# Performance work log

Measured on AMD Instinct MI355X. Metric: run time of the kernel, lower is better.

The kernel has to match this reference:

```python
import jax, jax.numpy as jnp
import numpy as np

T, B, M = 512, 4096, 2
DT = 1.0
HARD_RESET = True


def setup_inputs() -> dict:
    key = jax.random.key(0)
    ks = jax.random.split(key, 8)
    x_seq = jax.random.normal(ks[0], (T, B), jnp.float32) * 0.5
    w = jax.random.normal(ks[1], (B, B), jnp.float32) * (0.5 / np.sqrt(B))
    b = jax.random.normal(ks[2], (B,), jnp.float32) * 0.1
    v0 = jnp.zeros((B,), jnp.float32)
    Iasc0 = jnp.zeros((B, M), jnp.float32)
    v_th = jnp.ones((B,), jnp.float32)
    v_reset = jnp.zeros((B,), jnp.float32)
    v_rest = jnp.zeros((B,), jnp.float32)
    c_m = jnp.ones((B,), jnp.float32)
    tau = jax.random.uniform(ks[3], (B,), jnp.float32, 5.0, 20.0)
    k = jax.random.uniform(ks[4], (B, M), jnp.float32, 0.1, 0.5)
    asc = jax.random.normal(ks[5], (B, M), jnp.float32) * 0.1
    mask = jnp.ones((B,), jnp.float32)
    return dict(x_seq=x_seq, w=w, b=b, v0=v0, Iasc0=Iasc0, v_th=v_th,
                v_reset=v_reset, v_rest=v_rest, c_m=c_m, tau=tau, k=k,
                asc=asc, mask=mask)


def reference(x_seq, w, b, v0, Iasc0, v_th, v_reset, v_rest, c_m, tau, k, asc, mask):
    a = jnp.exp(-DT / tau)                 # (B,) voltage decay
    bdec = jnp.exp(-k * DT)                # (B,M) ASC decay

    def step(carry, x_t):
        v, I, s_prev = carry
        I_sum = I.sum(-1)                  # (B,)
        lin = w @ s_prev                   # recurrent GEMV against prev spikes
        x = x_t + b + lin
        v_inf = v_rest + tau * (x + I_sum) / c_m
        v_p = v_inf + (v - v_inf) * a
        u = (v_p - v_th) / (v_th - v_reset)
        s = (u > 0.0).astype(v_p.dtype) * mask
        if HARD_RESET:
            v_post = v_p - (v_p - v_reset) * s
        else:
            v_post = v_p - (v_th - v_reset) * s
        I_new = I * bdec + asc * s[:, None]
        return (v_post, I_new, s), (s, v_post)

    (v_fin, I_fin, _), (s_seq, v_seq) = jax.lax.scan(
        step, (v0, Iasc0, jnp.zeros_like(v0)), x_seq)
    return s_seq, v_seq, v_fin, I_fin
```

## Files before the change

kernel.cpp:

```cpp
#include <hip/hip_runtime.h>
#include <math.h>

#define TSTEPS 512
#define BN 4096
#define NBLK 64
#define NTHR 512
#define NPB 64
#define NWAVE 8
#define ESTRIDE 16

typedef unsigned long long u64;

__device__ __forceinline__ u64 ld_agent(const u64* p) {
    return __hip_atomic_load(p, __ATOMIC_RELAXED, __HIP_MEMORY_SCOPE_AGENT);
}
__device__ __forceinline__ void st_agent(u64* p, u64 v) {
    __hip_atomic_store(p, v, __ATOMIC_RELAXED, __HIP_MEMORY_SCOPE_AGENT);
}

template<bool TR>
__global__ __launch_bounds__(NTHR, 1)
void glif_kernel(const float* __restrict__ x_seq, const float* __restrict__ w,
                 const float* __restrict__ b_in, const float* __restrict__ v0,
                 const float* __restrict__ Ia0, const float* __restrict__ vth_in,
                 const float* __restrict__ vrst_in, const float* __restrict__ vrest_in,
                 const float* __restrict__ cm_in, const float* __restrict__ tau_in,
                 const float* __restrict__ k_in, const float* __restrict__ asc_in,
                 const float* __restrict__ mask_in,
                 float* __restrict__ out_s, float* __restrict__ out_v,
                 float* __restrict__ out_vf, float* __restrict__ out_if,
                 u64* __restrict__ sbuf, unsigned* __restrict__ bar,
                 float* __restrict__ wT)
{
    __shared__ float  tile[64][65];
    __shared__ int    wlist[NWAVE][512];
    __shared__ float4 partials[2][NWAVE][16];

    const int blk = blockIdx.x;
    const int tid = threadIdx.x;
    const int n0 = blk * NPB;
    const int wv = tid >> 6;
    const int ln = tid & 63;

    if (TR) {
        for (int tt = 0; tt < 64; ++tt) {
            int tile_id = blk + tt * NBLK;
            int ti = tile_id >> 6, tj = tile_id & 63;
            int c = tid & 63, r0 = tid >> 6;
#pragma unroll
            for (int rr = 0; rr < 8; ++rr) {
                int r = r0 + rr * 8;
                tile[r][c] = w[(size_t)(ti * 64 + r) * BN + tj * 64 + c];
            }
            __syncthreads();
            int rw = tid & 63, c0 = tid >> 6;
#pragma unroll
            for (int cc = 0; cc < 8; ++cc) {
                int cw = c0 + cc * 8;
                float mcol = mask_in[tj * 64 + cw];
                wT[(size_t)(tj * 64 + cw) * BN + ti * 64 + rw] = tile[rw][cw] * mcol;
            }
            __syncthreads();
        }
    }

    __syncthreads();
    if (tid == 0) {
        __threadfence();
        __hip_atomic_fetch_add(bar, 1u, __ATOMIC_ACQ_REL, __HIP_MEMORY_SCOPE_AGENT);
        while (__hip_atomic_load(bar, __ATOMIC_RELAXED, __HIP_MEMORY_SCOPE_AGENT) < NBLK) {
            __builtin_amdgcn_s_sleep(8);
        }
        __threadfence();
    }
    __syncthreads();

    const int n = n0 + tid;
    float v = 0, I0 = 0, I1 = 0, bb = 0, aa = 0, bd0 = 0, bd1 = 0, as0 = 0, as1 = 0,
          vth = 0, vrst = 0, vrest = 0, cm = 1, tau = 1, msk = 0;
    if (tid < NPB) {
        v = v0[n]; I0 = Ia0[2 * n]; I1 = Ia0[2 * n + 1];
        bb = b_in[n]; vth = vth_in[n]; vrst = vrst_in[n]; vrest = vrest_in[n];
        cm = cm_in[n]; tau = tau_in[n]; msk = mask_in[n];
        aa  = (float)exp((double)(-1.0f / tau));
        bd0 = (float)exp((double)(-k_in[2 * n]));
        bd1 = (float)exp((double)(-k_in[2 * n + 1]));
        as0 = asc_in[2 * n]; as1 = asc_in[2 * n + 1];
    }

    const int e = ln >> 3;
    const int sub = ln & 7;
    const int wsel = sub >> 2;
    const int bshift = 8 * (sub & 3);
    const int cbase = ((wv * 8 + e) << 6) + (sub << 3);

    const int cslot = ln >> 4, l16 = ln & 15;
    const float* wb4 = wT + n0 + l16 * 4;

    for (int t = 0; t < TSTEPS; ++t) {
        float xt = 0.0f;
        if (tid < NPB) xt = x_seq[(size_t)t * BN + n];

        const u64* p = sbuf + ((size_t)(t & 1) * NBLK + (wv * 8 + e)) * ESTRIDE + wsel;
        const unsigned want = (unsigned)t;
        u64 ev = ld_agent(p);
        while ((unsigned)(ev >> 32) != want) {
            __builtin_amdgcn_s_sleep(1);
            ev = ld_agent(p);
        }
        unsigned byte = ((unsigned)ev >> bshift) & 0xFFu;

        int c = __popc(byte);
        int x = c;
#pragma unroll
        for (int d = 1; d < 64; d <<= 1) {
            int y = __shfl_up(x, d);
            if (ln >= d) x += y;
        }
        const int kw = __shfl(x, 63);
        int base = x - c;
        while (byte) { int bp = __ffs(byte) - 1; byte &= byte - 1; wlist[wv][base++] = cbase + bp; }

        float4 acc = make_float4(0.f, 0.f, 0.f, 0.f);
        const int R = (kw + 3) >> 2;
        if (TR) {
            for (int r = 0; r < R; r += 8) {
#pragma unroll
                for (int u = 0; u < 8; ++u) {
                    int idx = (r + u) * 4 + cslot;
                    bool pg = idx < kw;
                    int j = wlist[wv][pg ? idx : 0];
                    float m = pg ? 1.0f : 0.0f;
                    const float4 wvv = *reinterpret_cast<const float4*>(wb4 + ((size_t)j << 12));
                    acc.x = fmaf(wvv.x, m, acc.x);
                    acc.y = fmaf(wvv.y, m, acc.y);
                    acc.z = fmaf(wvv.z, m, acc.z);
                    acc.w = fmaf(wvv.w, m, acc.w);
                }
            }
#pragma unroll
            for (int d = 16; d < 64; d <<= 1) {
                acc.x += __shfl_xor(acc.x, d);
                acc.y += __shfl_xor(acc.y, d);
                acc.z += __shfl_xor(acc.z, d);
                acc.w += __shfl_xor(acc.w, d);
            }
            if (ln < 16) partials[t & 1][wv][ln] = acc;
        } else {
            float accs = 0.f;
            const float* wrow = w + (size_t)(n0 + ln) * BN;
            for (int i = 0; i < kw; ++i) {
                int j = wlist[wv][i];
                accs = fmaf(wrow[j], mask_in[j], accs);
            }
            reinterpret_cast<float*>(&partials[t & 1][wv][0])[ln] = accs;
        }
        __syncthreads();

        float s = 0.0f;
        if (tid < NPB) {
            const float* pf = reinterpret_cast<const float*>(&partials[t & 1][0][0]);
            float l0 = pf[tid],        l1 = pf[64 + tid],  l2 = pf[128 + tid], l3 = pf[192 + tid];
            float l4 = pf[256 + tid],  l5 = pf[320 + tid], l6 = pf[384 + tid], l7 = pf[448 + tid];
            float lin = ((l0 + l1) + (l2 + l3)) + ((l4 + l5) + (l6 + l7));
            float xx = (xt + bb) + lin;
            float Isum = I0 + I1;
            float vinf = vrest + (tau * (xx + Isum)) / cm;
            float vp = vinf + (v - vinf) * aa;
            float uu = (vp - vth) / (vth - vrst);
            s = (uu > 0.0f) ? msk : 0.0f;
            u64 bal = __ballot(s != 0.0f);
            if (tid == 0) {
                u64 tagw = ((u64)(t + 1)) << 32;
                u64* dst = sbuf + ((size_t)((t + 1) & 1) * NBLK + blk) * ESTRIDE;
                st_agent(dst,     tagw | (u64)(unsigned)bal);
                st_agent(dst + 1, tagw | (u64)(unsigned)(bal >> 32));
            }
            float vpost = vp - (vp - vrst) * s;
            I0 = I0 * bd0 + as0 * s;
            I1 = I1 * bd1 + as1 * s;
            v = vpost;
            out_s[(size_t)t * BN + n] = s;
            out_v[(size_t)t * BN + n] = vpost;
        }
    }

    if (tid < NPB) {
        out_vf[n] = v;
        out_if[2 * n] = I0;
        out_if[2 * n + 1] = I1;
    }
}

extern "C" void kernel_launch(void* const* d_in, const int* in_sizes, int n_in,
                              void* d_out, int out_size, void* d_ws, size_t ws_size,
                              hipStream_t stream)
{
    const float* x_seq = (const float*)d_in[0];
    const float* w     = (const float*)d_in[1];
    const float* b     = (const float*)d_in[2];
    const float* v0    = (const float*)d_in[3];
    const float* Ia0   = (const float*)d_in[4];
    const float* vth   = (const float*)d_in[5];
    const float* vrst  = (const float*)d_in[6];
    const float* vrest = (const float*)d_in[7];
    const float* cm    = (const float*)d_in[8];
    const float* tau   = (const float*)d_in[9];
    const float* k     = (const float*)d_in[10];
    const float* asc   = (const float*)d_in[11];
    const float* mask  = (const float*)d_in[12];

    float* out_s  = (float*)d_out;
    float* out_v  = out_s + (size_t)TSTEPS * BN;
    float* out_vf = out_v + (size_t)TSTEPS * BN;
    float* out_if = out_vf + BN;

    const size_t mb_bytes = (size_t)2 * NBLK * ESTRIDE * sizeof(u64);
    u64* sbuf     = (u64*)d_ws;
    unsigned* bar = (unsigned*)((char*)d_ws + mb_bytes);
    float* wT     = (float*)((char*)d_ws + mb_bytes + 256);

    const size_t need = mb_bytes + 256 + (size_t)BN * BN * sizeof(float);
    const bool tr = (ws_size >= need);

    hipMemsetAsync(d_ws, 0, mb_bytes + 256, stream);

    if (tr) {
        glif_kernel<true><<<NBLK, NTHR, 0, stream>>>(
            x_seq, w, b, v0, Ia0, vth, vrst, vrest, cm, tau, k, asc, mask,
            out_s, out_v, out_vf, out_if, sbuf, bar, wT);
    } else {
        glif_kernel<false><<<NBLK, NTHR, 0, stream>>>(
            x_seq, w, b, v0, Ia0, vth, vrst, vrest, cm, tau, k, asc, mask,
            out_s, out_v, out_vf, out_if, sbuf, bar, (float*)w);
    }
}
```

Before: 1.708 ms.

## Split into a dedicated neuron-update wave and eight gather waves using LDS flags

Adds a ninth wave that owns the per-neuron state update and spike broadcast. The eight gather waves now signal completion through workgroup-scope release/acquire flags in LDS instead of a block-wide __syncthreads each timestep, and partials become a four-deep ring so gather waves can run ahead. The spin-wait on the global spike buffer also issues two loads per iteration with no sleep, to cut polling latency. The goal is to take the block barrier off the per-step critical path, at the cost of busy-spinning in LDS and in global memory.

```diff
diff --git a/kernel.cpp b/kernel.cpp
--- a/kernel.cpp
+++ b/kernel.cpp
@@ -4,9 +4,9 @@
 #define TSTEPS 512
 #define BN 4096
 #define NBLK 64
-#define NTHR 512
+#define NTHR 576
 #define NPB 64
-#define NWAVE 8
+#define NGW 8
 #define ESTRIDE 16
 
 typedef unsigned long long u64;
@@ -16,6 +16,12 @@
 }
 __device__ __forceinline__ void st_agent(u64* p, u64 v) {
     __hip_atomic_store(p, v, __ATOMIC_RELAXED, __HIP_MEMORY_SCOPE_AGENT);
+}
+__device__ __forceinline__ void st_flag(unsigned* p, unsigned v) {
+    __hip_atomic_store(p, v, __ATOMIC_RELEASE, __HIP_MEMORY_SCOPE_WORKGROUP);
+}
+__device__ __forceinline__ unsigned ld_flag(const unsigned* p) {
+    return __hip_atomic_load(p, __ATOMIC_ACQUIRE, __HIP_MEMORY_SCOPE_WORKGROUP);
 }
 
 template<bool TR>
@@ -32,9 +38,10 @@
                  u64* __restrict__ sbuf, unsigned* __restrict__ bar,
                  float* __restrict__ wT)
 {
-    __shared__ float  tile[64][65];
-    __shared__ int    wlist[NWAVE][512];
-    __shared__ float4 partials[2][NWAVE][16];
+    __shared__ float    tile[64][65];
+    __shared__ int      wlist[NGW][512];
+    __shared__ float4   partials[4][NGW][16];
+    __shared__ unsigned flags[NGW];
 
     const int blk = blockIdx.x;
     const int tid = threadIdx.x;
@@ -46,23 +53,29 @@
         for (int tt = 0; tt < 64; ++tt) {
             int tile_id = blk + tt * NBLK;
             int ti = tile_id >> 6, tj = tile_id & 63;
-            int c = tid & 63, r0 = tid >> 6;
-#pragma unroll
-            for (int rr = 0; rr < 8; ++rr) {
-                int r = r0 + rr * 8;
-                tile[r][c] = w[(size_t)(ti * 64 + r) * BN + tj * 64 + c];
+            if (tid < 512) {
+                int c = tid & 63, r0 = tid >> 6;
+#pragma unroll
+                for (int rr = 0; rr < 8; ++rr) {
+                    int r = r0 + rr * 8;
+                    tile[r][c] = w[(size_t)(ti * 64 + r) * BN + tj * 64 + c];
+                }
             }
             __syncthreads();
-            int rw = tid & 63, c0 = tid >> 6;
-#pragma unroll
-            for (int cc = 0; cc < 8; ++cc) {
-                int cw = c0 + cc * 8;
-                float mcol = mask_in[tj * 64 + cw];
-                wT[(size_t)(tj * 64 + cw) * BN + ti * 64 + rw] = tile[rw][cw] * mcol;
+            if (tid < 512) {
+                int rw = tid & 63, c0 = tid >> 6;
+#pragma unroll
+                for (int cc = 0; cc < 8; ++cc) {
+                    int cw = c0 + cc * 8;
+                    float mcol = mask_in[tj * 64 + cw];
+                    wT[(size_t)(tj * 64 + cw) * BN + ti * 64 + rw] = tile[rw][cw] * mcol;
+                }
             }
             __syncthreads();
         }
     }
+
+    if (tid < NGW) flags[tid] = 0;
 
     __syncthreads();
     if (tid == 0) {
@@ -75,10 +88,9 @@
     }
     __syncthreads();
 
-    const int n = n0 + tid;
-    float v = 0, I0 = 0, I1 = 0, bb = 0, aa = 0, bd0 = 0, bd1 = 0, as0 = 0, as1 = 0,
-          vth = 0, vrst = 0, vrest = 0, cm = 1, tau = 1, msk = 0;
-    if (tid < NPB) {
+    if (wv == 0) {
+        const int n = n0 + ln;
+        float v, I0, I1, bb, aa, bd0, bd1, as0, as1, vth, vrst, vrest, cm, tau, msk;
         v = v0[n]; I0 = Ia0[2 * n]; I1 = Ia0[2 * n + 1];
         bb = b_in[n]; vth = vth_in[n]; vrst = vrst_in[n]; vrest = vrest_in[n];
         cm = cm_in[n]; tau = tau_in[n]; msk = mask_in[n];
@@ -86,96 +98,28 @@
         bd0 = (float)exp((double)(-k_in[2 * n]));
         bd1 = (float)exp((double)(-k_in[2 * n + 1]));
         as0 = asc_in[2 * n]; as1 = asc_in[2 * n + 1];
-    }
-
-    const int e = ln >> 3;
-    const int sub = ln & 7;
-    const int wsel = sub >> 2;
-    const int bshift = 8 * (sub & 3);
-    const int cbase = ((wv * 8 + e) << 6) + (sub << 3);
-
-    const int cslot = ln >> 4, l16 = ln & 15;
-    const float* wb4 = wT + n0 + l16 * 4;
-
-    for (int t = 0; t < TSTEPS; ++t) {
-        float xt = 0.0f;
-        if (tid < NPB) xt = x_seq[(size_t)t * BN + n];
-
-        const u64* p = sbuf + ((size_t)(t & 1) * NBLK + (wv * 8 + e)) * ESTRIDE + wsel;
-        const unsigned want = (unsigned)t;
-        u64 ev = ld_agent(p);
-        while ((unsigned)(ev >> 32) != want) {
-            __builtin_amdgcn_s_sleep(1);
-            ev = ld_agent(p);
-        }
-        unsigned byte = ((unsigned)ev >> bshift) & 0xFFu;
-
-        int c = __popc(byte);
-        int x = c;
-#pragma unroll
-        for (int d = 1; d < 64; d <<= 1) {
-            int y = __shfl_up(x, d);
-            if (ln >= d) x += y;
-        }
-        const int kw = __shfl(x, 63);
-        int base = x - c;
-        while (byte) { int bp = __ffs(byte) - 1; byte &= byte - 1; wlist[wv][base++] = cbase + bp; }
-
-        float4 acc = make_float4(0.f, 0.f, 0.f, 0.f);
-        const int R = (kw + 3) >> 2;
-        if (TR) {
-            for (int r = 0; r < R; r += 8) {
-#pragma unroll
-                for (int u = 0; u < 8; ++u) {
-                    int idx = (r + u) * 4 + cslot;
-                    bool pg = idx < kw;
-                    int j = wlist[wv][pg ? idx : 0];
-                    float m = pg ? 1.0f : 0.0f;
-                    const float4 wvv = *reinterpret_cast<const float4*>(wb4 + ((size_t)j << 12));
-                    acc.x = fmaf(wvv.x, m, acc.x);
-                    acc.y = fmaf(wvv.y, m, acc.y);
-                    acc.z = fmaf(wvv.z, m, acc.z);
-                    acc.w = fmaf(wvv.w, m, acc.w);
-                }
-            }
-#pragma unroll
-            for (int d = 16; d < 64; d <<= 1) {
-                acc.x += __shfl_xor(acc.x, d);
-                acc.y += __shfl_xor(acc.y, d);
-                acc.z += __shfl_xor(acc.z, d);
-                acc.w += __shfl_xor(acc.w, d);
-            }
-            if (ln < 16) partials[t & 1][wv][ln] = acc;
-        } else {
-            float accs = 0.f;
-            const float* wrow = w + (size_t)(n0 + ln) * BN;
-            for (int i = 0; i < kw; ++i) {
-                int j = wlist[wv][i];
-                accs = fmaf(wrow[j], mask_in[j], accs);
-            }
-            reinterpret_cast<float*>(&partials[t & 1][wv][0])[ln] = accs;
-        }
-        __syncthreads();
-
-        float s = 0.0f;
-        if (tid < NPB) {
-            const float* pf = reinterpret_cast<const float*>(&partials[t & 1][0][0]);
-            float l0 = pf[tid],        l1 = pf[64 + tid],  l2 = pf[128 + tid], l3 = pf[192 + tid];
-            float l4 = pf[256 + tid],  l5 = pf[320 + tid], l6 = pf[384 + tid], l7 = pf[448 + tid];
+
+        for (int t = 0; t < TSTEPS; ++t) {
+            float xt = x_seq[(size_t)t * BN + n];
+
+            if (ln < NGW) {
+                const unsigned want = (unsigned)(t + 1);
+                while (ld_flag(&flags[ln]) < want) {}
+            }
+            const float* pf = reinterpret_cast<const float*>(&partials[t & 3][0][0]);
+            float l0 = pf[ln],        l1 = pf[64 + ln],  l2 = pf[128 + ln], l3 = pf[192 + ln];
+            float l4 = pf[256 + ln],  l5 = pf[320 + ln], l6 = pf[384 + ln], l7 = pf[448 + ln];
             float lin = ((l0 + l1) + (l2 + l3)) + ((l4 + l5) + (l6 + l7));
             float xx = (xt + bb) + lin;
             float Isum = I0 + I1;
             float vinf = vrest + (tau * (xx + Isum)) / cm;
             float vp = vinf + (v - vinf) * aa;
             float uu = (vp - vth) / (vth - vrst);
-            s = (uu > 0.0f) ? msk : 0.0f;
+            float s = (uu > 0.0f) ? msk : 0.0f;
             u64 bal = __ballot(s != 0.0f);
-            if (tid == 0) {
-                u64 tagw = ((u64)(t + 1)) << 32;
-                u64* dst = sbuf + ((size_t)((t + 1) & 1) * NBLK + blk) * ESTRIDE;
-                st_agent(dst,     tagw | (u64)(unsigned)bal);
-                st_agent(dst + 1, tagw | (u64)(unsigned)(bal >> 32));
-            }
+            u64 tagw = ((u64)(t + 1)) << 32;
+            u64* dst = sbuf + ((size_t)((t + 1) & 1) * NBLK + blk) * ESTRIDE;
+            if (ln < 2) st_agent(dst + ln, tagw | (u64)(unsigned)(bal >> (32 * ln)));
             float vpost = vp - (vp - vrst) * s;
             I0 = I0 * bd0 + as0 * s;
             I1 = I1 * bd1 + as1 * s;
@@ -183,12 +127,79 @@
             out_s[(size_t)t * BN + n] = s;
             out_v[(size_t)t * BN + n] = vpost;
         }
-    }
-
-    if (tid < NPB) {
         out_vf[n] = v;
         out_if[2 * n] = I0;
         out_if[2 * n + 1] = I1;
+    } else {
+        const int gw = wv - 1;
+        const int e = ln >> 3;
+        const int sub = ln & 7;
+        const int wsel = sub >> 2;
+        const int bshift = 8 * (sub & 3);
+        const int entry = gw * 8 + e;
+        const int cbase = (entry << 6) + (sub << 3);
+        const int cslot = ln >> 4, l16 = ln & 15;
+        const float* wb4 = wT + n0 + l16 * 4;
+
+        for (int t = 0; t < TSTEPS; ++t) {
+            const u64* p = sbuf + ((size_t)(t & 1) * NBLK + entry) * ESTRIDE + wsel;
+            const unsigned want = (unsigned)t;
+            u64 ev;
+            for (;;) {
+                u64 A = ld_agent(p);
+                u64 B = ld_agent(p);
+                if ((unsigned)(A >> 32) == want) { ev = A; break; }
+                if ((unsigned)(B >> 32) == want) { ev = B; break; }
+            }
+            unsigned byte = ((unsigned)ev >> bshift) & 0xFFu;
+
+            int c = __popc(byte);
+            int x = c;
+#pragma unroll
+            for (int d = 1; d < 64; d <<= 1) {
+                int y = __shfl_up(x, d);
+                if (ln >= d) x += y;
+            }
+            const int kw = __shfl(x, 63);
+            int base = x - c;
+            while (byte) { int bp = __ffs(byte) - 1; byte &= byte - 1; wlist[gw][base++] = cbase + bp; }
+
+            if (TR) {
+                float4 acc = make_float4(0.f, 0.f, 0.f, 0.f);
+                const int R = (kw + 3) >> 2;
+                for (int r = 0; r < R; r += 8) {
+#pragma unroll
+                    for (int u = 0; u < 8; ++u) {
+                        int idx = (r + u) * 4 + cslot;
+                        bool pg = idx < kw;
+                        int j = wlist[gw][pg ? idx : 0];
+                        float m = pg ? 1.0f : 0.0f;
+                        const float4 wvv = *reinterpret_cast<const float4*>(wb4 + ((size_t)j << 12));
+                        acc.x = fmaf(wvv.x, m, acc.x);
+                        acc.y = fmaf(wvv.y, m, acc.y);
+                        acc.z = fmaf(wvv.z, m, acc.z);
+                        acc.w = fmaf(wvv.w, m, acc.w);
+                    }
+                }
+#pragma unroll
+                for (int d = 16; d < 64; d <<= 1) {
+                    acc.x += __shfl_xor(acc.x, d);
+                    acc.y += __shfl_xor(acc.y, d);
+                    acc.z += __shfl_xor(acc.z, d);
+                    acc.w += __shfl_xor(acc.w, d);
+                }
+                if (ln < 16) partials[t & 3][gw][ln] = acc;
+            } else {
+                float accs = 0.f;
+                const float* wrow = w + (size_t)(n0 + ln) * BN;
+                for (int i = 0; i < kw; ++i) {
+                    int j = wlist[gw][i];
+                    accs = fmaf(wrow[j], mask_in[j], accs);
+                }
+                reinterpret_cast<float*>(&partials[t & 3][gw][0])[ln] = accs;
+            }
+            if (ln == 0) st_flag(&flags[gw], (unsigned)(t + 1));
+        }
     }
 }
 
```

After: 1.656 ms. 1.03x faster.
